# Kernel optimization log

Hardware: AMD Instinct MI355X
Metric: run time of the kernel (lower is better)

The kernel has to match this reference:

```python
import jax, jax.numpy as jnp
import numpy as np

N, E, IN_DIM, HID = 8192, 65536, 128, 64
BN_EPS = 1e-5


def setup_inputs() -> dict:
    key = jax.random.key(0)
    ks = jax.random.split(key, 16)
    inp = {
        'h': jax.random.normal(ks[0], (N, IN_DIM), dtype=jnp.float32),
        'src': jax.random.randint(ks[1], (E,), 0, N, dtype=jnp.int32),
        'dst': jax.random.randint(ks[2], (E,), 0, N, dtype=jnp.int32),
        'proj1_w': jax.random.normal(ks[3], (HID * HID, IN_DIM), dtype=jnp.float32) * 0.02,
        'proj1_b': jax.random.normal(ks[4], (HID * HID,), dtype=jnp.float32) * 0.02,
        'proj2_w': jax.random.normal(ks[5], (HID, IN_DIM), dtype=jnp.float32) * 0.02,
        'proj2_b': jax.random.normal(ks[6], (HID,), dtype=jnp.float32) * 0.02,
        'conv_w': jax.random.normal(ks[7], (1, 2, 3), dtype=jnp.float32) * 0.2,
        'conv_b': jax.random.normal(ks[8], (1,), dtype=jnp.float32) * 0.2,
        'ep2_w': jax.random.normal(ks[9], (HID, IN_DIM), dtype=jnp.float32) * 0.02,
        'ep2_b': jax.random.normal(ks[10], (HID,), dtype=jnp.float32) * 0.02,
        'ep3_w': jax.random.normal(ks[11], (HID, HID), dtype=jnp.float32) * 0.02,
        'ep3_b': jax.random.normal(ks[12], (HID,), dtype=jnp.float32) * 0.02,
        'bn_gamma': jnp.ones((HID,), dtype=jnp.float32),
        'bn_beta': jnp.zeros((HID,), dtype=jnp.float32),
        'bn_mean': jnp.zeros((HID,), dtype=jnp.float32),
        'bn_var': jnp.ones((HID,), dtype=jnp.float32),
    }
    return inp


def reference(h, src, dst, proj1_w, proj1_b, proj2_w, proj2_b, conv_w, conv_b,
              ep2_w, ep2_b, ep3_w, ep3_b, bn_gamma, bn_beta, bn_mean, bn_var):
    # ---- local edge path: cat(src,dst) -> Conv1d(2->1,k3,p1) -> Linear ----
    edge = jnp.stack([h[src], h[dst]], axis=1)  # [E, 2, in_dim]
    conv = jax.lax.conv_general_dilated(
        edge, conv_w, window_strides=(1,), padding=[(1, 1)],
        dimension_numbers=('NCW', 'OIW', 'NCW'))  # [E, 1, in_dim]
    conv = conv + conv_b[None, :, None]
    lr_e_local = jnp.squeeze(conv, axis=1) @ ep2_w.T + ep2_b  # [E, hid]

    # ---- global edge path (SDDMM form of the dense NxN*hid mm) ----
    # torch: mm.view(N,hid,N).permute(0,2,1)[src,dst] == A[src] @ p2[dst]
    A = (h @ proj1_w.T + proj1_b).reshape(-1, HID, HID)  # [N, hid, hid]
    p2 = h @ proj2_w.T + proj2_b                          # [N, hid]
    lr_e_global = jnp.einsum('ejd,ed->ej', A[src], p2[dst])  # [E, hid]
    lr_e_global = lr_e_global @ ep3_w.T + ep3_b

    e = lr_e_local + lr_e_global
    # BatchNorm1d in eval mode (running stats), then ReLU; dropout is a no-op in eval.
    e = (e - bn_mean) * jax.lax.rsqrt(bn_var + BN_EPS) * bn_gamma + bn_beta
    return jax.nn.relu(e)
```

## Files before the change

### kernel.cpp

```cpp
#include <hip/hip_runtime.h>
#include <stdint.h>

#define NN   8192
#define EE   65536
#define IND  128
#define HID  64
#define NB   4096
#define BCAP 64

typedef __attribute__((ext_vector_type(8))) short short8;
typedef __attribute__((ext_vector_type(4))) float f32x4;
typedef _Float16 h8f __attribute__((ext_vector_type(8)));

__device__ __forceinline__ unsigned short f2bf(float f) {
  unsigned int x = __float_as_uint(f);
  x += 0x7fffu + ((x >> 16) & 1u);
  return (unsigned short)(x >> 16);
}
__device__ __forceinline__ unsigned short f2h(float v) {
  return __builtin_bit_cast(unsigned short, (_Float16)v);
}

#define GLOAD_LDS16(g, l) __builtin_amdgcn_global_load_lds( \
    (const __attribute__((address_space(1))) unsigned int*)(g), \
    (__attribute__((address_space(3))) unsigned int*)(l), 16, 0, 0)

__global__ __launch_bounds__(256) void k_prep(const float* __restrict__ h,
                                              const float* __restrict__ proj1_w,
                                              const float* __restrict__ proj1_b,
                                              const float* __restrict__ ep3_w,
                                              const float* __restrict__ proj2_w,
                                              const float* __restrict__ ep2_w,
                                              const float* __restrict__ ep2_b,
                                              const float* __restrict__ conv_w,
                                              const float* __restrict__ conv_b,
                                              const float* __restrict__ ep3_b,
                                              const float* __restrict__ bn_g,
                                              const float* __restrict__ bn_b,
                                              const float* __restrict__ bn_m,
                                              const float* __restrict__ bn_v,
                                              unsigned short* __restrict__ h_bf,
                                              int* __restrict__ cnt,
                                              unsigned short* __restrict__ Wp_bf,
                                              float* __restrict__ bp,
                                              unsigned short* __restrict__ Wn,
                                              float* __restrict__ consts) {
  __shared__ union {
    struct { float ep3t[64][65]; float Ps[64][128]; float p1bs[64]; } w;
    float red[256];
  } sm;
  const int b = blockIdx.x;
  const int t = threadIdx.x;
  if (b < 512) {
    if (b < 8) *(int4*)(cnt + (size_t)b * 1024 + t * 4) = make_int4(0, 0, 0, 0);
    const int idx = b * 256 + t;
    const float4* s = (const float4*)h + (size_t)idx * 2;
    float4 a = s[0], bb = s[1];
    uint4 p;
    p.x = (unsigned)f2bf(a.x) | ((unsigned)f2bf(a.y) << 16);
    p.y = (unsigned)f2bf(a.z) | ((unsigned)f2bf(a.w) << 16);
    p.z = (unsigned)f2bf(bb.x) | ((unsigned)f2bf(bb.y) << 16);
    p.w = (unsigned)f2bf(bb.z) | ((unsigned)f2bf(bb.w) << 16);
    *(uint4*)(h_bf + (size_t)idx * 8) = p;
  } else if (b < 576) {
    const int d = b - 512;
#pragma unroll
    for (int s = 0; s < 16; ++s) {
      int idx = s * 256 + t;
      sm.w.ep3t[idx & 63][idx >> 6] = ep3_w[idx];
    }
#pragma unroll
    for (int s = 0; s < 8; ++s) {
      int idx = s * 256 + t;
      int j = idx >> 5, kq = idx & 31;
      *(float4*)&sm.w.Ps[j][kq * 4] = *(const float4*)(proj1_w + (size_t)(j * 64 + d) * IND + kq * 4);
    }
    if (t < 64) sm.w.p1bs[t] = proj1_b[t * 64 + d];
    __syncthreads();
    const int i = t & 63, kq = t >> 6;
    float acc[32];
#pragma unroll
    for (int kk = 0; kk < 32; ++kk) acc[kk] = 0.f;
    for (int j = 0; j < 64; ++j) {
      float e = sm.w.ep3t[j][i];
#pragma unroll
      for (int k4 = 0; k4 < 8; ++k4) {
        float4 pv = *(const float4*)&sm.w.Ps[j][kq * 32 + k4 * 4];
        acc[k4 * 4 + 0] += e * pv.x; acc[k4 * 4 + 1] += e * pv.y;
        acc[k4 * 4 + 2] += e * pv.z; acc[k4 * 4 + 3] += e * pv.w;
      }
    }
    unsigned short* dstp = Wp_bf + (size_t)(i * 64 + d) * IND + kq * 32;
#pragma unroll
    for (int kk = 0; kk < 32; kk += 2) {
      unsigned int p = (unsigned)f2bf(acc[kk]) | ((unsigned)f2bf(acc[kk + 1]) << 16);
      *(unsigned int*)(dstp + kk) = p;
    }
    if (kq == 0) {
      float bsum = 0.f;
      for (int j = 0; j < 64; ++j) bsum += sm.w.ep3t[j][i] * sm.w.p1bs[j];
      bp[i * 64 + d] = bsum;
    }
  } else {
    const int i = b - 576;
    const int x = t & 127;
    float u = 0.f, v = 0.f;
    for (int k = 0; k < 3; ++k) {
      int w = x + 1 - k;
      if (w >= 0 && w < IND) {
        float e = ep2_w[i * IND + w];
        u += conv_w[k] * e;
        v += conv_w[3 + k] * e;
      }
    }
    Wn[(size_t)i * IND + x]         = f2bf(proj2_w[i * IND + x]);
    Wn[(size_t)(64 + i) * IND + x]  = f2bf(u);
    Wn[(size_t)(128 + i) * IND + x] = f2bf(v);
    sm.red[t] = ep2_w[i * IND + x];
    __syncthreads();
    for (int s = 128; s > 0; s >>= 1) {
      if (t < s) sm.red[t] += sm.red[t + s];
      __syncthreads();
    }
    if (t == 0) {
      float scale = bn_g[i] * rsqrtf(bn_v[i] + 1e-5f);
      float shift = bn_b[i] - bn_m[i] * scale;
      float cb = conv_b[0] * sm.red[0] * 0.5f + ep2_b[i] + ep3_b[i];
      consts[i] = scale;
      consts[64 + i] = shift;
      consts[128 + i] = cb;
    }
  }
}

__global__ __launch_bounds__(256) void k_mm(const unsigned short* __restrict__ hbf,
                                            const unsigned short* __restrict__ Wbf,
                                            const float* __restrict__ bp,
                                            const unsigned short* __restrict__ Wn,
                                            const float* __restrict__ proj2_b,
                                            const int* __restrict__ src,
                                            const int* __restrict__ dst,
                                            int* __restrict__ cnt,
                                            int2* __restrict__ bucket,
                                            unsigned short* __restrict__ Bm,
                                            unsigned short* __restrict__ pld,
                                            float* __restrict__ Ls32) {
  __shared__ unsigned char sm[65536];
  const int t = threadIdx.x;
  if (blockIdx.x < 2048) {
    unsigned char* smA = sm;
    unsigned char* smB = sm + 32768;
    const int n0 = (blockIdx.x & 31) * 128, m0 = (blockIdx.x >> 5) * 128;
    const unsigned short* gA = hbf + (size_t)m0 * IND;
    const unsigned short* gB = Wbf + (size_t)n0 * IND;
#pragma unroll
    for (int s = 0; s < 8; ++s) {
      int p = s * 256 + t;
      int gp = (p & ~15) | ((p ^ (p >> 4)) & 15);
      GLOAD_LDS16(gA + gp * 8, smA + p * 16);
      GLOAD_LDS16(gB + gp * 8, smB + p * 16);
    }
    __syncthreads();
    const int w = t >> 6, lane = t & 63;
    const int wr = w >> 1, wc = w & 1;
    const int lrow = lane & 15, quad = lane >> 4;
    f32x4 acc[4][4] = {};
#pragma unroll
    for (int ks = 0; ks < 4; ++ks) {
      short8 af[4], bfr[4];
#pragma unroll
      for (int a = 0; a < 4; ++a) {
        int row = wr * 64 + a * 16 + lrow;
        int chunk = (ks * 4 + quad) ^ (row & 15);
        af[a] = *(const short8*)(smA + row * 256 + chunk * 16);
      }
#pragma unroll
      for (int b = 0; b < 4; ++b) {
        int row = wc * 64 + b * 16 + lrow;
        int chunk = (ks * 4 + quad) ^ (row & 15);
        bfr[b] = *(const short8*)(smB + row * 256 + chunk * 16);
      }
#pragma unroll
      for (int a = 0; a < 4; ++a)
#pragma unroll
        for (int b = 0; b < 4; ++b)
          acc[a][b] = __builtin_amdgcn_mfma_f32_16x16x32_bf16(af[a], bfr[b], acc[a][b], 0, 0, 0);
    }
    float bv[4];
#pragma unroll
    for (int b = 0; b < 4; ++b) bv[b] = bp[n0 + wc * 64 + b * 16 + lrow];
    __syncthreads();
#pragma unroll
    for (int a = 0; a < 4; ++a) {
      int R0 = wr * 64 + a * 16 + quad * 4;
#pragma unroll
      for (int b = 0; b < 4; ++b) {
        int C = wc * 64 + b * 16 + lrow;
#pragma unroll
        for (int v = 0; v < 4; ++v)
          *(unsigned short*)(sm + (size_t)(R0 + v) * 272 + C * 2) = f2h(acc[a][b][v] + bv[b]);
      }
    }
    __syncthreads();
#pragma unroll
    for (int s = 0; s < 8; ++s) {
      int p = s * 256 + t;
      int row = p >> 4, q = p & 15;
      uint4 val = *(const uint4*)(sm + (size_t)row * 272 + q * 16);
      *(uint4*)(Bm + (size_t)(m0 + row) * NB + n0 + q * 8) = val;
    }
  } else if (blockIdx.x < 2176) {
    unsigned char* smA = sm;
    unsigned char* smW = sm + 16384;
    const int m0 = (blockIdx.x - 2048) * 64;
#pragma unroll
    for (int s = 0; s < 4; ++s) {
      int p = s * 256 + t;
      int row = p >> 4, c = p & 15;
      int cs = c ^ (row & 15);
      GLOAD_LDS16(hbf + (size_t)(m0 + row) * IND + cs * 8, smA + p * 16);
    }
#pragma unroll
    for (int s = 0; s < 12; ++s) {
      int p = s * 256 + t;
      int row = p >> 4, c = p & 15;
      int cs = c ^ (row & 15);
      GLOAD_LDS16(Wn + (size_t)row * IND + cs * 8, smW + p * 16);
    }
    __syncthreads();
    const int w = t >> 6, lane = t & 63;
    const int lrow = lane & 15, quad = lane >> 4;
    f32x4 acc[12] = {};
#pragma unroll
    for (int ks = 0; ks < 4; ++ks) {
      const int chunk = (ks * 4 + quad) ^ lrow;
      short8 af = *(const short8*)(smA + (w * 16 + lrow) * 256 + chunk * 16);
#pragma unroll
      for (int n = 0; n < 12; ++n) {
        short8 bfr = *(const short8*)(smW + (n * 16 + lrow) * 256 + chunk * 16);
        acc[n] = __builtin_amdgcn_mfma_f32_16x16x32_bf16(af, bfr, acc[n], 0, 0, 0);
      }
    }
    const int row0 = m0 + w * 16 + quad * 4;
#pragma unroll
    for (int n = 0; n < 12; ++n) {
      int col = n * 16 + lrow;
      if (n < 4) {
        float b = proj2_b[col];
#pragma unroll
        for (int v = 0; v < 4; ++v)
          pld[(size_t)(row0 + v) * 128 + col] = f2h(acc[n][v] + b);
      } else if (n < 8) {
        int c2 = col - 64;
#pragma unroll
        for (int v = 0; v < 4; ++v)
          Ls32[(size_t)(row0 + v) * HID + c2] = acc[n][v];
      } else {
        int c2 = col - 128;
#pragma unroll
        for (int v = 0; v < 4; ++v)
          pld[(size_t)(row0 + v) * 128 + 64 + c2] = f2h(acc[n][v]);
      }
    }
  } else {
    const int e = (blockIdx.x - 2176) * 256 + t;
    const int s = src[e], d = dst[e];
    const int p = atomicAdd(&cnt[s], 1);
    if (p < BCAP) bucket[(size_t)s * BCAP + p] = make_int2(e, d);
  }
}

__global__ __launch_bounds__(256) void k_edge(const int* __restrict__ cnt,
                                              const int2* __restrict__ bucket,
                                              const unsigned short* __restrict__ Bm,
                                              const unsigned short* __restrict__ pld,
                                              const float* __restrict__ Ls32,
                                              const float* __restrict__ consts,
                                              float* __restrict__ out) {
  const int t = threadIdx.x;
  const int w = t >> 6, lane = t & 63;
  const int s = blockIdx.x * 4 + w;
  const int n = min(cnt[s], BCAP);
  if (n == 0) return;
  const int lrow = lane & 15, quad = lane >> 4;
  const unsigned short* Brow = Bm + (size_t)s * NB;
  h8f afr[4][2];
#pragma unroll
  for (int tt = 0; tt < 4; ++tt)
#pragma unroll
    for (int ks = 0; ks < 2; ++ks)
      afr[tt][ks] = *(const h8f*)(Brow + (tt * 16 + lrow) * 64 + ks * 32 + quad * 8);
  h8f idf[4];
#pragma unroll
  for (int tt = 0; tt < 4; ++tt) {
    int j = tt * 16 + lrow - (tt >> 1) * 32 - quad * 8;
    uint4 iw = make_uint4(0, 0, 0, 0);
    if (j >= 0 && j < 8) {
      unsigned val = 0x3C00u << ((j & 1) * 16);
      int jw = j >> 1;
      if (jw == 0) iw.x = val; else if (jw == 1) iw.y = val;
      else if (jw == 2) iw.z = val; else iw.w = val;
    }
    idf[tt] = __builtin_bit_cast(h8f, iw);
  }
  float4 sc4[4], sh4[4], cbl[4];
#pragma unroll
  for (int tt = 0; tt < 4; ++tt) {
    int ib = tt * 16 + quad * 4;
    sc4[tt] = *(const float4*)(consts + ib);
    sh4[tt] = *(const float4*)(consts + 64 + ib);
    float4 cb = *(const float4*)(consts + 128 + ib);
    float4 ls = *(const float4*)(Ls32 + (size_t)s * HID + ib);
    cbl[tt] = make_float4(cb.x + ls.x, cb.y + ls.y, cb.z + ls.z, cb.w + ls.w);
  }
  for (int b0 = 0; b0 < n; b0 += 16) {
    const int idx = b0 + lrow;
    const int2 ed = bucket[(size_t)s * BCAP + min(idx, n - 1)];
    const unsigned short* prow = pld + (size_t)ed.y * 128;
    h8f bf0 = *(const h8f*)(prow + quad * 8);
    h8f bf1 = *(const h8f*)(prow + 32 + quad * 8);
    h8f bl0 = *(const h8f*)(prow + 64 + quad * 8);
    h8f bl1 = *(const h8f*)(prow + 96 + quad * 8);
    f32x4 acc[4] = {};
#pragma unroll
    for (int tt = 0; tt < 4; ++tt) {
      acc[tt] = __builtin_amdgcn_mfma_f32_16x16x32_f16(afr[tt][0], bf0, acc[tt], 0, 0, 0);
      acc[tt] = __builtin_amdgcn_mfma_f32_16x16x32_f16(afr[tt][1], bf1, acc[tt], 0, 0, 0);
      acc[tt] = __builtin_amdgcn_mfma_f32_16x16x32_f16(idf[tt], (tt < 2) ? bl0 : bl1, acc[tt], 0, 0, 0);
    }
    if (idx < n) {
      float* orow = out + (size_t)ed.x * HID;
#pragma unroll
      for (int tt = 0; tt < 4; ++tt) {
        float4 o;
        o.x = fmaxf((acc[tt][0] + cbl[tt].x) * sc4[tt].x + sh4[tt].x, 0.f);
        o.y = fmaxf((acc[tt][1] + cbl[tt].y) * sc4[tt].y + sh4[tt].y, 0.f);
        o.z = fmaxf((acc[tt][2] + cbl[tt].z) * sc4[tt].z + sh4[tt].z, 0.f);
        o.w = fmaxf((acc[tt][3] + cbl[tt].w) * sc4[tt].w + sh4[tt].w, 0.f);
        *(float4*)(orow + tt * 16 + quad * 4) = o;
      }
    }
  }
}

extern "C" void kernel_launch(void* const* d_in, const int* in_sizes, int n_in,
                              void* d_out, int out_size, void* d_ws, size_t ws_size,
                              hipStream_t stream) {
  const float* h       = (const float*)d_in[0];
  const int*   src     = (const int*)d_in[1];
  const int*   dst     = (const int*)d_in[2];
  const float* proj1_w = (const float*)d_in[3];
  const float* proj1_b = (const float*)d_in[4];
  const float* proj2_w = (const float*)d_in[5];
  const float* proj2_b = (const float*)d_in[6];
  const float* conv_w  = (const float*)d_in[7];
  const float* conv_b  = (const float*)d_in[8];
  const float* ep2_w   = (const float*)d_in[9];
  const float* ep2_b   = (const float*)d_in[10];
  const float* ep3_w   = (const float*)d_in[11];
  const float* ep3_b   = (const float*)d_in[12];
  const float* bn_g    = (const float*)d_in[13];
  const float* bn_b    = (const float*)d_in[14];
  const float* bn_m    = (const float*)d_in[15];
  const float* bn_v    = (const float*)d_in[16];

  char* ws = (char*)d_ws;
  unsigned short* Wp_bf = (unsigned short*)ws;  ws += (size_t)NB * IND * 2;
  unsigned short* h_bf  = (unsigned short*)ws;  ws += (size_t)NN * IND * 2;
  float* bp     = (float*)ws;                   ws += (size_t)NB * 4;
  unsigned short* Wn = (unsigned short*)ws;     ws += (size_t)192 * IND * 2;
  float* consts = (float*)ws;                   ws += 1024;
  int* cnt      = (int*)ws;                     ws += 8192 * 4;
  int2* bucket  = (int2*)ws;                    ws += (size_t)NN * BCAP * 8;
  unsigned short* pld = (unsigned short*)ws;    ws += (size_t)NN * 128 * 2;
  float* Ls32   = (float*)ws;                   ws += (size_t)NN * HID * 4;
  unsigned short* Bm = (unsigned short*)ws;

  k_prep<<<640, 256, 0, stream>>>(h, proj1_w, proj1_b, ep3_w, proj2_w,
                                  ep2_w, ep2_b, conv_w, conv_b, ep3_b,
                                  bn_g, bn_b, bn_m, bn_v,
                                  h_bf, cnt, Wp_bf, bp, Wn, consts);
  k_mm<<<2432, 256, 0, stream>>>(h_bf, Wp_bf, bp, Wn, proj2_b, src, dst,
                                 cnt, bucket, Bm, pld, Ls32);
  k_edge<<<NN / 4, 256, 0, stream>>>(cnt, bucket, Bm, pld, Ls32, consts, (float*)d_out);
}
```

Measured before the change: 160.9 us.

## Fuse per-node A-matrix GEMM into edge kernel, drop Bm global buffer

The big N x 4096 projection GEMM is no longer written to a global fp16 buffer (Bm, about 64 MB) and read back. Each block of the edge kernel now computes the A matrices for its 16 source nodes directly into LDS, in two halves of 2048 columns, and consumes them immediately for the SDDMM edge work. This removes a large global write and read round trip. In exchange, the weight matrix is re-read from global/L2 by every block with less reuse, the fused kernel uses 64 KB of LDS (lower occupancy), and edge work per half is serialized behind the GEMM.

```diff
diff --git a/kernel.cpp b/kernel.cpp
--- a/kernel.cpp
+++ b/kernel.cpp
@@ -133,86 +133,21 @@
   }
 }
 
-__global__ __launch_bounds__(256) void k_mm(const unsigned short* __restrict__ hbf,
-                                            const unsigned short* __restrict__ Wbf,
-                                            const float* __restrict__ bp,
-                                            const unsigned short* __restrict__ Wn,
-                                            const float* __restrict__ proj2_b,
-                                            const int* __restrict__ src,
-                                            const int* __restrict__ dst,
-                                            int* __restrict__ cnt,
-                                            int2* __restrict__ bucket,
-                                            unsigned short* __restrict__ Bm,
-                                            unsigned short* __restrict__ pld,
-                                            float* __restrict__ Ls32) {
+__global__ __launch_bounds__(256) void k_mid(const unsigned short* __restrict__ hbf,
+                                             const unsigned short* __restrict__ Wn,
+                                             const float* __restrict__ proj2_b,
+                                             const int* __restrict__ src,
+                                             const int* __restrict__ dst,
+                                             int* __restrict__ cnt,
+                                             int2* __restrict__ bucket,
+                                             unsigned short* __restrict__ pld,
+                                             float* __restrict__ Ls32) {
   __shared__ unsigned char sm[65536];
   const int t = threadIdx.x;
-  if (blockIdx.x < 2048) {
-    unsigned char* smA = sm;
-    unsigned char* smB = sm + 32768;
-    const int n0 = (blockIdx.x & 31) * 128, m0 = (blockIdx.x >> 5) * 128;
-    const unsigned short* gA = hbf + (size_t)m0 * IND;
-    const unsigned short* gB = Wbf + (size_t)n0 * IND;
-#pragma unroll
-    for (int s = 0; s < 8; ++s) {
-      int p = s * 256 + t;
-      int gp = (p & ~15) | ((p ^ (p >> 4)) & 15);
-      GLOAD_LDS16(gA + gp * 8, smA + p * 16);
-      GLOAD_LDS16(gB + gp * 8, smB + p * 16);
-    }
-    __syncthreads();
-    const int w = t >> 6, lane = t & 63;
-    const int wr = w >> 1, wc = w & 1;
-    const int lrow = lane & 15, quad = lane >> 4;
-    f32x4 acc[4][4] = {};
-#pragma unroll
-    for (int ks = 0; ks < 4; ++ks) {
-      short8 af[4], bfr[4];
-#pragma unroll
-      for (int a = 0; a < 4; ++a) {
-        int row = wr * 64 + a * 16 + lrow;
-        int chunk = (ks * 4 + quad) ^ (row & 15);
-        af[a] = *(const short8*)(smA + row * 256 + chunk * 16);
-      }
-#pragma unroll
-      for (int b = 0; b < 4; ++b) {
-        int row = wc * 64 + b * 16 + lrow;
-        int chunk = (ks * 4 + quad) ^ (row & 15);
-        bfr[b] = *(const short8*)(smB + row * 256 + chunk * 16);
-      }
-#pragma unroll
-      for (int a = 0; a < 4; ++a)
-#pragma unroll
-        for (int b = 0; b < 4; ++b)
-          acc[a][b] = __builtin_amdgcn_mfma_f32_16x16x32_bf16(af[a], bfr[b], acc[a][b], 0, 0, 0);
-    }
-    float bv[4];
-#pragma unroll
-    for (int b = 0; b < 4; ++b) bv[b] = bp[n0 + wc * 64 + b * 16 + lrow];
-    __syncthreads();
-#pragma unroll
-    for (int a = 0; a < 4; ++a) {
-      int R0 = wr * 64 + a * 16 + quad * 4;
-#pragma unroll
-      for (int b = 0; b < 4; ++b) {
-        int C = wc * 64 + b * 16 + lrow;
-#pragma unroll
-        for (int v = 0; v < 4; ++v)
-          *(unsigned short*)(sm + (size_t)(R0 + v) * 272 + C * 2) = f2h(acc[a][b][v] + bv[b]);
-      }
-    }
-    __syncthreads();
-#pragma unroll
-    for (int s = 0; s < 8; ++s) {
-      int p = s * 256 + t;
-      int row = p >> 4, q = p & 15;
-      uint4 val = *(const uint4*)(sm + (size_t)row * 272 + q * 16);
-      *(uint4*)(Bm + (size_t)(m0 + row) * NB + n0 + q * 8) = val;
-    }
-  } else if (blockIdx.x < 2176) {
+  if (blockIdx.x < 128) {
     unsigned char* smA = sm;
     unsigned char* smW = sm + 16384;
-    const int m0 = (blockIdx.x - 2048) * 64;
+    const int m0 = blockIdx.x * 64;
 #pragma unroll
     for (int s = 0; s < 4; ++s) {
       int p = s * 256 + t;
@@ -263,37 +198,35 @@
       }
     }
   } else {
-    const int e = (blockIdx.x - 2176) * 256 + t;
+    const int e = (blockIdx.x - 128) * 256 + t;
     const int s = src[e], d = dst[e];
     const int p = atomicAdd(&cnt[s], 1);
     if (p < BCAP) bucket[(size_t)s * BCAP + p] = make_int2(e, d);
   }
 }
 
-__global__ __launch_bounds__(256) void k_edge(const int* __restrict__ cnt,
-                                              const int2* __restrict__ bucket,
-                                              const unsigned short* __restrict__ Bm,
-                                              const unsigned short* __restrict__ pld,
-                                              const float* __restrict__ Ls32,
-                                              const float* __restrict__ consts,
-                                              float* __restrict__ out) {
+__global__ __launch_bounds__(256) void k_fused(const unsigned short* __restrict__ hbf,
+                                               const unsigned short* __restrict__ Wbf,
+                                               const float* __restrict__ bp,
+                                               const int* __restrict__ cnt,
+                                               const int2* __restrict__ bucket,
+                                               const unsigned short* __restrict__ pld,
+                                               const float* __restrict__ Ls32,
+                                               const float* __restrict__ consts,
+                                               float* __restrict__ out) {
+  __shared__ unsigned char At[65536];
   const int t = threadIdx.x;
   const int w = t >> 6, lane = t & 63;
-  const int s = blockIdx.x * 4 + w;
-  const int n = min(cnt[s], BCAP);
-  if (n == 0) return;
   const int lrow = lane & 15, quad = lane >> 4;
-  const unsigned short* Brow = Bm + (size_t)s * NB;
-  h8f afr[4][2];
-#pragma unroll
-  for (int tt = 0; tt < 4; ++tt)
-#pragma unroll
-    for (int ks = 0; ks < 2; ++ks)
-      afr[tt][ks] = *(const h8f*)(Brow + (tt * 16 + lrow) * 64 + ks * 32 + quad * 8);
-  h8f idf[4];
-#pragma unroll
-  for (int tt = 0; tt < 4; ++tt) {
-    int j = tt * 16 + lrow - (tt >> 1) * 32 - quad * 8;
+  const int s0 = blockIdx.x * 16;
+  short8 hf[4];
+#pragma unroll
+  for (int ks = 0; ks < 4; ++ks)
+    hf[ks] = *(const short8*)(hbf + (size_t)(s0 + lrow) * IND + ks * 32 + quad * 8);
+  h8f idf[2];
+#pragma unroll
+  for (int tt = 0; tt < 2; ++tt) {
+    int j = tt * 16 + lrow - quad * 8;
     uint4 iw = make_uint4(0, 0, 0, 0);
     if (j >= 0 && j < 8) {
       unsigned val = 0x3C00u << ((j & 1) * 16);
@@ -303,41 +236,84 @@
     }
     idf[tt] = __builtin_bit_cast(h8f, iw);
   }
-  float4 sc4[4], sh4[4], cbl[4];
-#pragma unroll
-  for (int tt = 0; tt < 4; ++tt) {
-    int ib = tt * 16 + quad * 4;
-    sc4[tt] = *(const float4*)(consts + ib);
-    sh4[tt] = *(const float4*)(consts + 64 + ib);
-    float4 cb = *(const float4*)(consts + 128 + ib);
-    float4 ls = *(const float4*)(Ls32 + (size_t)s * HID + ib);
-    cbl[tt] = make_float4(cb.x + ls.x, cb.y + ls.y, cb.z + ls.z, cb.w + ls.w);
-  }
-  for (int b0 = 0; b0 < n; b0 += 16) {
-    const int idx = b0 + lrow;
-    const int2 ed = bucket[(size_t)s * BCAP + min(idx, n - 1)];
-    const unsigned short* prow = pld + (size_t)ed.y * 128;
-    h8f bf0 = *(const h8f*)(prow + quad * 8);
-    h8f bf1 = *(const h8f*)(prow + 32 + quad * 8);
-    h8f bl0 = *(const h8f*)(prow + 64 + quad * 8);
-    h8f bl1 = *(const h8f*)(prow + 96 + quad * 8);
-    f32x4 acc[4] = {};
-#pragma unroll
-    for (int tt = 0; tt < 4; ++tt) {
-      acc[tt] = __builtin_amdgcn_mfma_f32_16x16x32_f16(afr[tt][0], bf0, acc[tt], 0, 0, 0);
-      acc[tt] = __builtin_amdgcn_mfma_f32_16x16x32_f16(afr[tt][1], bf1, acc[tt], 0, 0, 0);
-      acc[tt] = __builtin_amdgcn_mfma_f32_16x16x32_f16(idf[tt], (tt < 2) ? bl0 : bl1, acc[tt], 0, 0, 0);
-    }
-    if (idx < n) {
-      float* orow = out + (size_t)ed.x * HID;
-#pragma unroll
-      for (int tt = 0; tt < 4; ++tt) {
-        float4 o;
-        o.x = fmaxf((acc[tt][0] + cbl[tt].x) * sc4[tt].x + sh4[tt].x, 0.f);
-        o.y = fmaxf((acc[tt][1] + cbl[tt].y) * sc4[tt].y + sh4[tt].y, 0.f);
-        o.z = fmaxf((acc[tt][2] + cbl[tt].z) * sc4[tt].z + sh4[tt].z, 0.f);
-        o.w = fmaxf((acc[tt][3] + cbl[tt].w) * sc4[tt].w + sh4[tt].w, 0.f);
-        *(float4*)(orow + tt * 16 + quad * 4) = o;
+  int ncnt[4];
+#pragma unroll
+  for (int q = 0; q < 4; ++q) ncnt[q] = min(cnt[s0 + w * 4 + q], BCAP);
+
+  for (int hh = 0; hh < 2; ++hh) {
+    if (hh) __syncthreads();
+    const int rbase = hh * 2048 + w * 512;
+    for (int nt = 0; nt < 32; ++nt) {
+      const int r = rbase + nt * 16;
+      const unsigned short* wr = Wbf + (size_t)(r + lrow) * IND + quad * 8;
+      short8 a0 = *(const short8*)(wr);
+      short8 a1 = *(const short8*)(wr + 32);
+      short8 a2 = *(const short8*)(wr + 64);
+      short8 a3 = *(const short8*)(wr + 96);
+      f32x4 acc = {};
+      acc = __builtin_amdgcn_mfma_f32_16x16x32_bf16(a0, hf[0], acc, 0, 0, 0);
+      acc = __builtin_amdgcn_mfma_f32_16x16x32_bf16(a1, hf[1], acc, 0, 0, 0);
+      acc = __builtin_amdgcn_mfma_f32_16x16x32_bf16(a2, hf[2], acc, 0, 0, 0);
+      acc = __builtin_amdgcn_mfma_f32_16x16x32_bf16(a3, hf[3], acc, 0, 0, 0);
+      float4 bv = *(const float4*)(bp + r + quad * 4);
+      const int rl = w * 512 + nt * 16 + quad * 4;
+      const int key = (rl >> 6) & 7;
+      const int cw = (rl >> 3) ^ key;
+      unsigned u0 = (unsigned)f2h(acc[0] + bv.x) | ((unsigned)f2h(acc[1] + bv.y) << 16);
+      unsigned u1 = (unsigned)f2h(acc[2] + bv.z) | ((unsigned)f2h(acc[3] + bv.w) << 16);
+      *(uint2*)(At + lrow * 4096 + (cw << 4) + (quad & 1) * 8) = make_uint2(u0, u1);
+    }
+    __syncthreads();
+    for (int q = 0; q < 4; ++q) {
+      const int n = ncnt[q];
+      if (n == 0) continue;
+      const int sl = w * 4 + q;
+      const int s  = s0 + sl;
+      h8f afr[2][2];
+#pragma unroll
+      for (int tt = 0; tt < 2; ++tt)
+#pragma unroll
+        for (int ks = 0; ks < 2; ++ks) {
+          int il = tt * 16 + lrow;
+          int c = (il * 8 + ks * 4 + quad) ^ (il & 7);
+          afr[tt][ks] = *(const h8f*)(At + sl * 4096 + c * 16);
+        }
+      float4 sc4[2], sh4[2], cbl[2];
+#pragma unroll
+      for (int tt = 0; tt < 2; ++tt) {
+        int ib = hh * 32 + tt * 16 + quad * 4;
+        sc4[tt] = *(const float4*)(consts + ib);
+        sh4[tt] = *(const float4*)(consts + 64 + ib);
+        float4 cb = *(const float4*)(consts + 128 + ib);
+        float4 ls = *(const float4*)(Ls32 + (size_t)s * HID + ib);
+        cbl[tt] = make_float4(cb.x + ls.x, cb.y + ls.y, cb.z + ls.z, cb.w + ls.w);
+      }
+      for (int b0 = 0; b0 < n; b0 += 16) {
+        const int idx = b0 + lrow;
+        const int2 ed = bucket[(size_t)s * BCAP + min(idx, n - 1)];
+        const unsigned short* prow = pld + (size_t)ed.y * 128;
+        h8f bf0 = *(const h8f*)(prow + quad * 8);
+        h8f bf1 = *(const h8f*)(prow + 32 + quad * 8);
+        h8f bl  = *(const h8f*)(prow + 64 + hh * 32 + quad * 8);
+        f32x4 a2[2] = {};
+#pragma unroll
+        for (int tt = 0; tt < 2; ++tt) {
+          a2[tt] = __builtin_amdgcn_mfma_f32_16x16x32_f16(afr[tt][0], bf0, a2[tt], 0, 0, 0);
+          a2[tt] = __builtin_amdgcn_mfma_f32_16x16x32_f16(afr[tt][1], bf1, a2[tt], 0, 0, 0);
+          a2[tt] = __builtin_amdgcn_mfma_f32_16x16x32_f16(idf[tt], bl, a2[tt], 0, 0, 0);
+        }
+        if (idx < n) {
+          float* orow = out + (size_t)ed.x * HID + hh * 32;
+#pragma unroll
+          for (int tt = 0; tt < 2; ++tt) {
+            float4 o;
+            o.x = fmaxf((a2[tt][0] + cbl[tt].x) * sc4[tt].x + sh4[tt].x, 0.f);
+            o.y = fmaxf((a2[tt][1] + cbl[tt].y) * sc4[tt].y + sh4[tt].y, 0.f);
+            o.z = fmaxf((a2[tt][2] + cbl[tt].z) * sc4[tt].z + sh4[tt].z, 0.f);
+            o.w = fmaxf((a2[tt][3] + cbl[tt].w) * sc4[tt].w + sh4[tt].w, 0.f);
+            *(float4*)(orow + tt * 16 + quad * 4) = o;
+          }
+        }
       }
     }
   }
@@ -374,13 +350,12 @@
   int2* bucket  = (int2*)ws;                    ws += (size_t)NN * BCAP * 8;
   unsigned short* pld = (unsigned short*)ws;    ws += (size_t)NN * 128 * 2;
   float* Ls32   = (float*)ws;                   ws += (size_t)NN * HID * 4;
-  unsigned short* Bm = (unsigned short*)ws;
 
   k_prep<<<640, 256, 0, stream>>>(h, proj1_w, proj1_b, ep3_w, proj2_w,
                                   ep2_w, ep2_b, conv_w, conv_b, ep3_b,
                                   bn_g, bn_b, bn_m, bn_v,
                                   h_bf, cnt, Wp_bf, bp, Wn, consts);
-  k_mm<<<2432, 256, 0, stream>>>(h_bf, Wp_bf, bp, Wn, proj2_b, src, dst,
-                                 cnt, bucket, Bm, pld, Ls32);
-  k_edge<<<NN / 4, 256, 0, stream>>>(cnt, bucket, Bm, pld, Ls32, consts, (float*)d_out);
-}
+  k_mid<<<384, 256, 0, stream>>>(h_bf, Wn, proj2_b, src, dst, cnt, bucket, pld, Ls32);
+  k_fused<<<NN / 16, 256, 0, stream>>>(h_bf, Wp_bf, bp, cnt, bucket, pld, Ls32,
+                                       consts, (float*)d_out);
+}
```

Result: slower. 198.2 us (+23.2%).
